# Performance work log

Measured on AMD Instinct MI355X. Metric: run time of the kernel, lower is better.

## Reference

```python
import jax, jax.numpy as jnp
import numpy as np

S = 256 * 256  # imwidth * imheight = self.s
B = 1024       # batch size


def setup_inputs() -> dict:
    key = jax.random.key(0)
    k1, k2, k3 = jax.random.split(key, 3)
    z = jax.random.normal(k1, (B, S), dtype=jnp.float32)
    # Single TT core for N=1: shape (ranklist[0], s, ranklist[1]) = (1, S, 1)
    W = jax.random.normal(k2, (1, S, 1), dtype=jnp.float32) * 0.01
    # Bias parameter self.b, shape (s,)
    bias = jax.random.normal(k3, (S,), dtype=jnp.float32) * 0.01
    return {"z": z, "W": W, "bias": bias, "b": B}


def reference(z, W, bias, b):
    # Faithful N=1 forward of PolyclassFTTlayer_seq, without the redundant
    # zero-padded V scatter:
    #   V[:, :, 0, 0, 0] = z @ W.reshape(S, 1)          -> scalar per batch row
    #   f = W[0] (S, 1);  f @ V -> (b, 1, S, 1)
    #   out = f.reshape(b, S) / 1!  + bias
    # i.e. out[i, :] = (z[i] . w) * w + bias, with w = W[0, :, 0].
    w = W[0, :, 0]                     # (S,)
    scal = z @ w                       # (b,)  memory-bound matvec
    return scal[:, None] * w[None, :] + bias  # (b, S) outer product + bias
```

## Files before the change

### kernel.cpp

```cpp
#include <hip/hip_runtime.h>


#define SDIM 65536
#define S4   16384
#define BLK  512

typedef float floatx4 __attribute__((ext_vector_type(4)));

__device__ __forceinline__ float dot4(floatx4 a, floatx4 b) {
    return a.x * b.x + a.y * b.y + a.z * b.z + a.w * b.w;
}

__global__ __launch_bounds__(BLK) void dot2_kernel(
    const float* __restrict__ z,
    const float* __restrict__ w,
    float* __restrict__ scal)
{
    const int r0 = blockIdx.x * 2;
    const floatx4* __restrict__ z0 =
        reinterpret_cast<const floatx4*>(z + (size_t)r0 * SDIM);
    const floatx4* __restrict__ z1 =
        reinterpret_cast<const floatx4*>(z + (size_t)(r0 + 1) * SDIM);
    const floatx4* __restrict__ w4 = reinterpret_cast<const floatx4*>(w);

    float a00 = 0.f, a01 = 0.f, a02 = 0.f, a03 = 0.f;
    float a10 = 0.f, a11 = 0.f, a12 = 0.f, a13 = 0.f;
    for (int i = threadIdx.x; i < S4; i += 4 * BLK) {
        floatx4 y0 = w4[i];
        floatx4 y1 = w4[i + BLK];
        floatx4 y2 = w4[i + 2 * BLK];
        floatx4 y3 = w4[i + 3 * BLK];
        floatx4 p0 = z0[i];
        floatx4 p1 = z0[i + BLK];
        floatx4 p2 = z0[i + 2 * BLK];
        floatx4 p3 = z0[i + 3 * BLK];
        floatx4 q0 = z1[i];
        floatx4 q1 = z1[i + BLK];
        floatx4 q2 = z1[i + 2 * BLK];
        floatx4 q3 = z1[i + 3 * BLK];
        a00 += dot4(p0, y0); a01 += dot4(p1, y1);
        a02 += dot4(p2, y2); a03 += dot4(p3, y3);
        a10 += dot4(q0, y0); a11 += dot4(q1, y1);
        a12 += dot4(q2, y2); a13 += dot4(q3, y3);
    }
    float accA = (a00 + a01) + (a02 + a03);
    float accB = (a10 + a11) + (a12 + a13);

    #pragma unroll
    for (int off = 32; off > 0; off >>= 1) {
        accA += __shfl_down(accA, off, 64);
        accB += __shfl_down(accB, off, 64);
    }

    __shared__ float smem[BLK / 64][2];
    const int lane = threadIdx.x & 63;
    const int wid  = threadIdx.x >> 6;
    if (lane == 0) { smem[wid][0] = accA; smem[wid][1] = accB; }
    __syncthreads();
    if (threadIdx.x == 0) {
        float t0 = 0.f, t1 = 0.f;
        #pragma unroll
        for (int i = 0; i < BLK / 64; ++i) { t0 += smem[i][0]; t1 += smem[i][1]; }
        scal[r0]     = t0;
        scal[r0 + 1] = t1;
    }
}

#define OBLK   256
#define ORROWS 4
#define NCHUNK 4
#define CHUNK4 (S4 / NCHUNK)

__global__ __launch_bounds__(OBLK) void outer4_kernel(
    const float* __restrict__ scal,
    const float* __restrict__ w,
    const float* __restrict__ bias,
    float* __restrict__ out)
{
    const int group = blockIdx.x >> 2;
    const int chunk = blockIdx.x & (NCHUNK - 1);
    const int r0    = group * ORROWS;
    const int base  = chunk * CHUNK4;

    const float s0 = scal[r0];
    const float s1 = scal[r0 + 1];
    const float s2 = scal[r0 + 2];
    const float s3 = scal[r0 + 3];

    const floatx4* __restrict__ w4 = reinterpret_cast<const floatx4*>(w) + base;
    const floatx4* __restrict__ b4 = reinterpret_cast<const floatx4*>(bias) + base;
    floatx4* __restrict__ o0 =
        reinterpret_cast<floatx4*>(out + (size_t)r0 * SDIM) + base;
    floatx4* __restrict__ o1 =
        reinterpret_cast<floatx4*>(out + (size_t)(r0 + 1) * SDIM) + base;
    floatx4* __restrict__ o2 =
        reinterpret_cast<floatx4*>(out + (size_t)(r0 + 2) * SDIM) + base;
    floatx4* __restrict__ o3 =
        reinterpret_cast<floatx4*>(out + (size_t)(r0 + 3) * SDIM) + base;

    for (int i = threadIdx.x; i < CHUNK4; i += 2 * OBLK) {
        floatx4 y0 = w4[i];
        floatx4 y1 = w4[i + OBLK];
        floatx4 c0 = b4[i];
        floatx4 c1 = b4[i + OBLK];

        floatx4 t;
        t.x = fmaf(s0, y0.x, c0.x); t.y = fmaf(s0, y0.y, c0.y);
        t.z = fmaf(s0, y0.z, c0.z); t.w = fmaf(s0, y0.w, c0.w);
        __builtin_nontemporal_store(t, &o0[i]);
        t.x = fmaf(s1, y0.x, c0.x); t.y = fmaf(s1, y0.y, c0.y);
        t.z = fmaf(s1, y0.z, c0.z); t.w = fmaf(s1, y0.w, c0.w);
        __builtin_nontemporal_store(t, &o1[i]);
        t.x = fmaf(s2, y0.x, c0.x); t.y = fmaf(s2, y0.y, c0.y);
        t.z = fmaf(s2, y0.z, c0.z); t.w = fmaf(s2, y0.w, c0.w);
        __builtin_nontemporal_store(t, &o2[i]);
        t.x = fmaf(s3, y0.x, c0.x); t.y = fmaf(s3, y0.y, c0.y);
        t.z = fmaf(s3, y0.z, c0.z); t.w = fmaf(s3, y0.w, c0.w);
        __builtin_nontemporal_store(t, &o3[i]);

        t.x = fmaf(s0, y1.x, c1.x); t.y = fmaf(s0, y1.y, c1.y);
        t.z = fmaf(s0, y1.z, c1.z); t.w = fmaf(s0, y1.w, c1.w);
        __builtin_nontemporal_store(t, &o0[i + OBLK]);
        t.x = fmaf(s1, y1.x, c1.x); t.y = fmaf(s1, y1.y, c1.y);
        t.z = fmaf(s1, y1.z, c1.z); t.w = fmaf(s1, y1.w, c1.w);
        __builtin_nontemporal_store(t, &o1[i + OBLK]);
        t.x = fmaf(s2, y1.x, c1.x); t.y = fmaf(s2, y1.y, c1.y);
        t.z = fmaf(s2, y1.z, c1.z); t.w = fmaf(s2, y1.w, c1.w);
        __builtin_nontemporal_store(t, &o2[i + OBLK]);
        t.x = fmaf(s3, y1.x, c1.x); t.y = fmaf(s3, y1.y, c1.y);
        t.z = fmaf(s3, y1.z, c1.z); t.w = fmaf(s3, y1.w, c1.w);
        __builtin_nontemporal_store(t, &o3[i + OBLK]);
    }
}

extern "C" void kernel_launch(void* const* d_in, const int* in_sizes, int n_in,
                              void* d_out, int out_size, void* d_ws, size_t ws_size,
                              hipStream_t stream)
{
    const float* z    = (const float*)d_in[0];
    const float* w    = (const float*)d_in[1];
    const float* bias = (const float*)d_in[2];
    float* out  = (float*)d_out;
    float* scal = (float*)d_ws;

    const int B = in_sizes[0] / SDIM;

    dot2_kernel<<<B / 2, BLK, 0, stream>>>(z, w, scal);
    outer4_kernel<<<(B / ORROWS) * NCHUNK, OBLK, 0, stream>>>(scal, w, bias, out);
}
```

Before: 93.91 us.

## Fuse dot-product and outer-product kernels into one per-row-pair kernel

Merges the matvec reduction and the outer-product+bias write into a single kernel. Each block computes the scalars for two rows, shares them through LDS, then writes those two output rows. This removes the second launch, the workspace round-trip and the inter-kernel serialization, and lets reads and writes from different blocks overlap. In exchange the write phase has less parallelism per block (two rows, 512 blocks) than the previous finer-grained outer kernel.

```diff
diff --git a/kernel.cpp b/kernel.cpp
--- a/kernel.cpp
+++ b/kernel.cpp
@@ -11,10 +11,11 @@
     return a.x * b.x + a.y * b.y + a.z * b.z + a.w * b.w;
 }
 
-__global__ __launch_bounds__(BLK) void dot2_kernel(
+__global__ __launch_bounds__(BLK) void fused2_kernel(
     const float* __restrict__ z,
     const float* __restrict__ w,
-    float* __restrict__ scal)
+    const float* __restrict__ bias,
+    float* __restrict__ out)
 {
     const int r0 = blockIdx.x * 2;
     const floatx4* __restrict__ z0 =
@@ -22,6 +23,11 @@
     const floatx4* __restrict__ z1 =
         reinterpret_cast<const floatx4*>(z + (size_t)(r0 + 1) * SDIM);
     const floatx4* __restrict__ w4 = reinterpret_cast<const floatx4*>(w);
+    const floatx4* __restrict__ b4 = reinterpret_cast<const floatx4*>(bias);
+    floatx4* __restrict__ o0 =
+        reinterpret_cast<floatx4*>(out + (size_t)r0 * SDIM);
+    floatx4* __restrict__ o1 =
+        reinterpret_cast<floatx4*>(out + (size_t)(r0 + 1) * SDIM);
 
     float a00 = 0.f, a01 = 0.f, a02 = 0.f, a03 = 0.f;
     float a10 = 0.f, a11 = 0.f, a12 = 0.f, a13 = 0.f;
@@ -53,57 +59,27 @@
     }
 
     __shared__ float smem[BLK / 64][2];
+    __shared__ float sb[2];
     const int lane = threadIdx.x & 63;
     const int wid  = threadIdx.x >> 6;
     if (lane == 0) { smem[wid][0] = accA; smem[wid][1] = accB; }
     __syncthreads();
-    if (threadIdx.x == 0) {
-        float t0 = 0.f, t1 = 0.f;
+    if (threadIdx.x < 2) {
+        const int r = threadIdx.x;
+        float t = 0.f;
         #pragma unroll
-        for (int i = 0; i < BLK / 64; ++i) { t0 += smem[i][0]; t1 += smem[i][1]; }
-        scal[r0]     = t0;
-        scal[r0 + 1] = t1;
+        for (int i = 0; i < BLK / 64; ++i) t += smem[i][r];
+        sb[r] = t;
     }
-}
+    __syncthreads();
+    const float s0 = sb[0];
+    const float s1 = sb[1];
 
-#define OBLK   256
-#define ORROWS 4
-#define NCHUNK 4
-#define CHUNK4 (S4 / NCHUNK)
-
-__global__ __launch_bounds__(OBLK) void outer4_kernel(
-    const float* __restrict__ scal,
-    const float* __restrict__ w,
-    const float* __restrict__ bias,
-    float* __restrict__ out)
-{
-    const int group = blockIdx.x >> 2;
-    const int chunk = blockIdx.x & (NCHUNK - 1);
-    const int r0    = group * ORROWS;
-    const int base  = chunk * CHUNK4;
-
-    const float s0 = scal[r0];
-    const float s1 = scal[r0 + 1];
-    const float s2 = scal[r0 + 2];
-    const float s3 = scal[r0 + 3];
-
-    const floatx4* __restrict__ w4 = reinterpret_cast<const floatx4*>(w) + base;
-    const floatx4* __restrict__ b4 = reinterpret_cast<const floatx4*>(bias) + base;
-    floatx4* __restrict__ o0 =
-        reinterpret_cast<floatx4*>(out + (size_t)r0 * SDIM) + base;
-    floatx4* __restrict__ o1 =
-        reinterpret_cast<floatx4*>(out + (size_t)(r0 + 1) * SDIM) + base;
-    floatx4* __restrict__ o2 =
-        reinterpret_cast<floatx4*>(out + (size_t)(r0 + 2) * SDIM) + base;
-    floatx4* __restrict__ o3 =
-        reinterpret_cast<floatx4*>(out + (size_t)(r0 + 3) * SDIM) + base;
-
-    for (int i = threadIdx.x; i < CHUNK4; i += 2 * OBLK) {
+    for (int i = threadIdx.x; i < S4; i += 2 * BLK) {
         floatx4 y0 = w4[i];
-        floatx4 y1 = w4[i + OBLK];
+        floatx4 y1 = w4[i + BLK];
         floatx4 c0 = b4[i];
-        floatx4 c1 = b4[i + OBLK];
-
+        floatx4 c1 = b4[i + BLK];
         floatx4 t;
         t.x = fmaf(s0, y0.x, c0.x); t.y = fmaf(s0, y0.y, c0.y);
         t.z = fmaf(s0, y0.z, c0.z); t.w = fmaf(s0, y0.w, c0.w);
@@ -111,25 +87,12 @@
         t.x = fmaf(s1, y0.x, c0.x); t.y = fmaf(s1, y0.y, c0.y);
         t.z = fmaf(s1, y0.z, c0.z); t.w = fmaf(s1, y0.w, c0.w);
         __builtin_nontemporal_store(t, &o1[i]);
-        t.x = fmaf(s2, y0.x, c0.x); t.y = fmaf(s2, y0.y, c0.y);
-        t.z = fmaf(s2, y0.z, c0.z); t.w = fmaf(s2, y0.w, c0.w);
-        __builtin_nontemporal_store(t, &o2[i]);
-        t.x = fmaf(s3, y0.x, c0.x); t.y = fmaf(s3, y0.y, c0.y);
-        t.z = fmaf(s3, y0.z, c0.z); t.w = fmaf(s3, y0.w, c0.w);
-        __builtin_nontemporal_store(t, &o3[i]);
-
         t.x = fmaf(s0, y1.x, c1.x); t.y = fmaf(s0, y1.y, c1.y);
         t.z = fmaf(s0, y1.z, c1.z); t.w = fmaf(s0, y1.w, c1.w);
-        __builtin_nontemporal_store(t, &o0[i + OBLK]);
+        __builtin_nontemporal_store(t, &o0[i + BLK]);
         t.x = fmaf(s1, y1.x, c1.x); t.y = fmaf(s1, y1.y, c1.y);
         t.z = fmaf(s1, y1.z, c1.z); t.w = fmaf(s1, y1.w, c1.w);
-        __builtin_nontemporal_store(t, &o1[i + OBLK]);
-        t.x = fmaf(s2, y1.x, c1.x); t.y = fmaf(s2, y1.y, c1.y);
-        t.z = fmaf(s2, y1.z, c1.z); t.w = fmaf(s2, y1.w, c1.w);
-        __builtin_nontemporal_store(t, &o2[i + OBLK]);
-        t.x = fmaf(s3, y1.x, c1.x); t.y = fmaf(s3, y1.y, c1.y);
-        t.z = fmaf(s3, y1.z, c1.z); t.w = fmaf(s3, y1.w, c1.w);
-        __builtin_nontemporal_store(t, &o3[i + OBLK]);
+        __builtin_nontemporal_store(t, &o1[i + BLK]);
     }
 }
 
@@ -140,11 +103,9 @@
     const float* z    = (const float*)d_in[0];
     const float* w    = (const float*)d_in[1];
     const float* bias = (const float*)d_in[2];
-    float* out  = (float*)d_out;
-    float* scal = (float*)d_ws;
+    float* out = (float*)d_out;
 
     const int B = in_sizes[0] / SDIM;
 
-    dot2_kernel<<<B / 2, BLK, 0, stream>>>(z, w, scal);
-    outer4_kernel<<<(B / ORROWS) * NCHUNK, OBLK, 0, stream>>>(scal, w, bias, out);
+    fused2_kernel<<<B / 2, BLK, 0, stream>>>(z, w, bias, out);
 }
```

Measured after the change: 95.89 us. +2.1%, slower.
